# Kernel optimization log

Hardware: AMD Instinct MI355X
Metric: run time of the kernel (lower is better)

Reference implementation:

```python
import jax, jax.numpy as jnp
import numpy as np

IMG_W, IMG_H = 640, 480
OS = 8            # roialign output_size
SCALE = 1.0       # spatial_scale (boxes already mapped to feature coords)
ALIGNED = True
ALPHA = 1.0       # student-t alpha


def _roi_align_one(feat, boxes):
    # feat: [C, H, W]; boxes: [sn, 4] (x1, y1, x2, y2) in feature coords.
    # torchvision RoIAlign, sampling_ratio=1 (one sample at each bin center).
    C, H, W = feat.shape
    off = 0.5 if ALIGNED else 0.0
    x1 = boxes[:, 0] * SCALE - off
    y1 = boxes[:, 1] * SCALE - off
    x2 = boxes[:, 2] * SCALE - off
    y2 = boxes[:, 3] * SCALE - off
    bw = (x2 - x1) / OS   # bin width  [sn]
    bh = (y2 - y1) / OS   # bin height [sn]
    grid = jnp.arange(OS, dtype=feat.dtype) + 0.5
    xs = x1[:, None] + grid * bw[:, None]   # [sn, OS]
    ys = y1[:, None] + grid * bh[:, None]   # [sn, OS]
    X = jnp.broadcast_to(xs[:, None, :], (xs.shape[0], OS, OS))  # [sn,OS,OS]
    Y = jnp.broadcast_to(ys[:, :, None], (ys.shape[0], OS, OS))
    valid = (Y >= -1.0) & (Y <= H) & (X >= -1.0) & (X <= W)
    y = jnp.clip(Y, 0.0, H - 1)
    x = jnp.clip(X, 0.0, W - 1)
    y0f = jnp.floor(y); x0f = jnp.floor(x)
    y0 = y0f.astype(jnp.int32); x0 = x0f.astype(jnp.int32)
    y1i = jnp.minimum(y0 + 1, H - 1); x1i = jnp.minimum(x0 + 1, W - 1)
    ly = y - y0f; lx = x - x0f
    hy = 1.0 - ly; hx = 1.0 - lx
    def g(yi, xi):
        return feat[:, yi, xi]  # [C, sn, OS, OS]
    val = (hy * hx)[None] * g(y0, x0) + (hy * lx)[None] * g(y0, x1i) \
        + (ly * hx)[None] * g(y1i, x0) + (ly * lx)[None] * g(y1i, x1i)
    val = jnp.where(valid[None], val, 0.0)
    return jnp.transpose(val, (1, 0, 2, 3))  # [sn, C, OS, OS]


def setup_inputs() -> dict:
    key = jax.random.key(0)
    ks = jax.random.split(key, 10)
    B, SN, C, T, FY, FX = 16, 64, 480, 2, 60, 80
    NDF1, NDF2, K = 1024, 256, 64
    z = jax.random.normal(ks[0], (B, C, T, FY, FX), jnp.float32)
    # boxes in image pixel coords
    cx = jax.random.uniform(ks[1], (B, SN), minval=0.1, maxval=0.9) * IMG_W
    cy = jax.random.uniform(ks[2], (B, SN), minval=0.1, maxval=0.9) * IMG_H
    bw = jax.random.uniform(ks[3], (B, SN), minval=0.05, maxval=0.3) * IMG_W
    bh = jax.random.uniform(ks[4], (B, SN), minval=0.05, maxval=0.3) * IMG_H
    x1 = jnp.clip(cx - bw / 2, 0.0, IMG_W); x2 = jnp.clip(cx + bw / 2, 0.0, IMG_W)
    y1 = jnp.clip(cy - bh / 2, 0.0, IMG_H); y2 = jnp.clip(cy + bh / 2, 0.0, IMG_H)
    bboxs = jnp.stack([x1, y1, x2, y2], axis=-1).astype(jnp.float32)
    din = C * OS * OS
    w1 = jax.random.normal(ks[5], (NDF1, din), jnp.float32) * (din ** -0.5)
    b1 = jnp.zeros((NDF1,), jnp.float32)
    w2 = jax.random.normal(ks[6], (NDF2, NDF1), jnp.float32) * (NDF1 ** -0.5)
    b2 = jnp.zeros((NDF2,), jnp.float32)
    centroids = jax.random.normal(ks[7], (K, NDF2), jnp.float32)
    return {"z": z, "bboxs": bboxs, "w1": w1, "b1": b1, "w2": w2, "b2": b2,
            "centroids": centroids}


def reference(z, bboxs, w1, b1, w2, b2, centroids):
    B, C, T, fy, fx = z.shape
    sn = bboxs.shape[1]
    # scale image-space boxes to feature coords (per (x,y) pair as in torch code)
    sc = jnp.array([fx / IMG_W, fy / IMG_H], jnp.float32)
    bb = (bboxs.reshape(B, sn, 2, 2) * sc).reshape(B, sn, 4)
    bb = jnp.nan_to_num(bb)
    feat = z[:, :, -1]  # [B, C, fy, fx]
    pooled = jax.vmap(_roi_align_one)(feat, bb)  # [B, sn, C, OS, OS]
    flat = pooled.reshape(B * sn, -1)
    e = flat @ w1.T + b1
    e = e @ w2.T + b2
    zz = e.reshape(B, sn, -1)  # [B, sn, ndf2]
    # student-t soft assignment (faithful: L2 norm, not squared)
    z2 = jnp.sum(zz * zz, axis=-1, keepdims=True)          # [B,sn,1]
    c2 = jnp.sum(centroids * centroids, axis=-1)           # [K]
    zc = jnp.einsum('bsd,kd->bsk', zz, centroids)          # [B,sn,K]
    nrm = jnp.sqrt(jnp.maximum(z2 + c2 - 2.0 * zc, 0.0))
    s = ((1.0 + nrm) / ALPHA) ** (-(ALPHA + 1.0) / 2.0)
    s = s / jnp.sum(s, axis=-1, keepdims=True)
    c = jnp.argmax(s, axis=2)
    return zz, s, c
```

## Files before the change

### kernel.cpp

```cpp
#include <hip/hip_runtime.h>
#include <hip/hip_bf16.h>

static constexpr int B_  = 16;
static constexpr int SN_ = 64;
static constexpr int C_  = 480;
static constexpr int T_  = 2;
static constexpr int FY_ = 60;
static constexpr int FX_ = 80;
static constexpr int OS_ = 8;
static constexpr int DIN = 30720;
static constexpr int M_  = 1024;
static constexpr int N1_ = 1024;
static constexpr int N2_ = 256;
static constexpr int K_  = 64;
static constexpr int SPLITK = 32;
static constexpr int NCH_ZZ = (DIN / 64) / SPLITK;
static constexpr int NCH_FW = N1_ / 64;
static constexpr int CPB = 2;
static constexpr int IMG = FY_ * FX_;
static constexpr int NB_ROI = 16 * (C_ / CPB);
static constexpr int NB_W1T = (DIN / 64) * (N1_ / 64);
static constexpr int NB_W2P = N2_;

typedef __bf16 bf16x8 __attribute__((ext_vector_type(8)));
typedef float  f32x4  __attribute__((ext_vector_type(4)));
typedef unsigned int u32_as1 __attribute__((address_space(1)));
typedef unsigned int u32_as3 __attribute__((address_space(3)));

__device__ __forceinline__ float bf2f(unsigned short u) {
    union { unsigned int i; float f; } v; v.i = ((unsigned int)u) << 16; return v.f;
}
__device__ __forceinline__ unsigned short f2bf(float f) {
    unsigned int u = __float_as_uint(f);
    u = u + 0x7FFFu + ((u >> 16) & 1u);
    return (unsigned short)(u >> 16);
}
__device__ __forceinline__ void gll16(const void* g, void* l) {
    __builtin_amdgcn_global_load_lds((const u32_as1*)g, (u32_as3*)l, 16, 0, 0);
}

template<int NCHUNK, int SEG>
__device__ __forceinline__ void gemm_core(
    const unsigned short* __restrict__ Abase, long long Astride,
    const unsigned short* __restrict__ Bbase, long long Bstride,
    int k0, f32x4 (&acc)[4][2], unsigned short* L)
{
    const int t = threadIdx.x;
    const int w = t >> 6, lane = t & 63;
    const int rl8 = lane >> 3, slot = lane & 7;
    const int wm = w >> 2, wn = w & 3;
    const int fr = lane & 15, fg = lane >> 4;
    const int swz8 = (slot ^ rl8) * 8;

    long long arow[2], brow[2];
    int ci[2];
#pragma unroll
    for (int c = 0; c < 2; ++c) {
        ci[c] = w * 2 + c;
        const int row = ci[c] * 8 + rl8;
        arow[c] = (long long)row * Astride;
        brow[c] = (long long)row * Bstride;
    }

    auto stage = [&](int chunk, int par) {
        const int kin = k0 + chunk * 64;
        char* Lp = (char*)L + par * 65536;
#pragma unroll
        for (int c = 0; c < 2; ++c) {
            gll16(Abase + arow[c] + kin + swz8,       Lp + 0 * 16384 + ci[c] * 1024);
            gll16(Abase + arow[c] + SEG + kin + swz8, Lp + 1 * 16384 + ci[c] * 1024);
            gll16(Bbase + brow[c] + kin + swz8,       Lp + 2 * 16384 + ci[c] * 1024);
            gll16(Bbase + brow[c] + SEG + kin + swz8, Lp + 3 * 16384 + ci[c] * 1024);
        }
    };

    stage(0, 0);
    stage(1, 1);

    for (int it = 0; it < NCHUNK; ++it) {
        const int par = it & 1;
        if (it + 1 < NCHUNK) asm volatile("s_waitcnt vmcnt(8)" ::: "memory");
        else                 asm volatile("s_waitcnt vmcnt(0)" ::: "memory");
        __builtin_amdgcn_s_barrier();

        const char* Lp = (const char*)L + par * 65536;
        bf16x8 a[2][2][4], b[2][2][2];
#pragma unroll
        for (int hl = 0; hl < 2; ++hl)
#pragma unroll
            for (int ks = 0; ks < 2; ++ks)
#pragma unroll
                for (int mf = 0; mf < 4; ++mf) {
                    const int row = wm * 64 + mf * 16 + fr;
                    a[hl][ks][mf] = *reinterpret_cast<const bf16x8*>(
                        Lp + hl * 16384 + row * 128 + 16 * ((ks * 4 + fg) ^ (fr & 7)));
                }
#pragma unroll
        for (int hl = 0; hl < 2; ++hl)
#pragma unroll
            for (int ks = 0; ks < 2; ++ks)
#pragma unroll
                for (int nf = 0; nf < 2; ++nf) {
                    const int row = wn * 32 + nf * 16 + fr;
                    b[hl][ks][nf] = *reinterpret_cast<const bf16x8*>(
                        Lp + (2 + hl) * 16384 + row * 128 + 16 * ((ks * 4 + fg) ^ (fr & 7)));
                }
        asm volatile("s_waitcnt lgkmcnt(0)" ::: "memory");
        __builtin_amdgcn_sched_barrier(0);
        __builtin_amdgcn_s_barrier();
        __builtin_amdgcn_sched_barrier(0);
        if (it + 2 < NCHUNK) stage(it + 2, par);
        __builtin_amdgcn_sched_barrier(0);

        __builtin_amdgcn_s_setprio(1);
#pragma unroll
        for (int ks = 0; ks < 2; ++ks)
#pragma unroll
            for (int mf = 0; mf < 4; ++mf)
#pragma unroll
                for (int nf = 0; nf < 2; ++nf) {
                    acc[mf][nf] = __builtin_amdgcn_mfma_f32_16x16x32_bf16(
                        a[0][ks][mf], b[0][ks][nf], acc[mf][nf], 0, 0, 0);
                    acc[mf][nf] = __builtin_amdgcn_mfma_f32_16x16x32_bf16(
                        a[0][ks][mf], b[1][ks][nf], acc[mf][nf], 0, 0, 0);
                    acc[mf][nf] = __builtin_amdgcn_mfma_f32_16x16x32_bf16(
                        a[1][ks][mf], b[0][ks][nf], acc[mf][nf], 0, 0, 0);
                }
        __builtin_amdgcn_s_setprio(0);
    }
}

__global__ __launch_bounds__(256) void prep_kernel(
    const float* __restrict__ z, const float* __restrict__ bboxs,
    const float* __restrict__ w1, const float* __restrict__ w2,
    const float* __restrict__ b1, const float* __restrict__ b2,
    unsigned short* __restrict__ flat2, unsigned short* __restrict__ w1T2,
    unsigned short* __restrict__ w2cat, float* __restrict__ bf) {
    __shared__ __align__(16) char smem[39424];
    const int blk = blockIdx.x;
    const int t = threadIdx.x;

    if (blk < NB_ROI) {
        float* img = (float*)smem;
        float (*bxc)[4] = (float (*)[4])(smem + 38400);
        const int b  = blk / (C_ / CPB);
        const int cg = blk % (C_ / CPB);
        const float* zb = z + ((size_t)b * C_ + (size_t)cg * CPB) * (size_t)(T_ * IMG)
                            + (size_t)(T_ - 1) * IMG;
#pragma unroll
        for (int c = 0; c < CPB; ++c) {
            const float4* src = (const float4*)(zb + (size_t)c * (T_ * IMG));
            float4* dst = (float4*)(img + c * IMG);
            for (int i = t; i < IMG / 4; i += 256) dst[i] = src[i];
        }
        if (t < 64) {
            const float* bp = bboxs + ((size_t)b * 64 + t) * 4;
            const float v0 = bp[0], v1 = bp[1], v2 = bp[2], v3 = bp[3];
            bxc[t][0] = isnan(v0) ? 0.f : v0;
            bxc[t][1] = isnan(v1) ? 0.f : v1;
            bxc[t][2] = isnan(v2) ? 0.f : v2;
            bxc[t][3] = isnan(v3) ? 0.f : v3;
        }
        __syncthreads();

        const int p = t & 63, mh = t >> 6;
        const int gy = p >> 3, gx = p & 7;
        for (int mq = 0; mq < 16; ++mq) {
            const int m = mq * 4 + mh;
            const float x1 = bxc[m][0] * 0.125f - 0.5f;
            const float y1 = bxc[m][1] * 0.125f - 0.5f;
            const float x2 = bxc[m][2] * 0.125f - 0.5f;
            const float y2 = bxc[m][3] * 0.125f - 0.5f;
            const float bw = (x2 - x1) * (1.0f / OS_);
            const float bh = (y2 - y1) * (1.0f / OS_);
            const float X = x1 + ((float)gx + 0.5f) * bw;
            const float Y = y1 + ((float)gy + 0.5f) * bh;
            const bool valid = (Y >= -1.0f) && (Y <= (float)FY_) &&
                               (X >= -1.0f) && (X <= (float)FX_);
            const float yc = fminf(fmaxf(Y, 0.f), (float)(FY_ - 1));
            const float xc = fminf(fmaxf(X, 0.f), (float)(FX_ - 1));
            const float y0f = floorf(yc), x0f = floorf(xc);
            const int y0 = (int)y0f, x0 = (int)x0f;
            const int y1i = min(y0 + 1, FY_ - 1);
            const int x1i = min(x0 + 1, FX_ - 1);
            const float ly = yc - y0f, lx = xc - x0f;
            const float hy = 1.f - ly,  hx = 1.f - lx;
            float w00 = hy * hx, w01 = hy * lx, w10 = ly * hx, w11 = ly * lx;
            if (!valid) { w00 = 0.f; w01 = 0.f; w10 = 0.f; w11 = 0.f; }
            const int i00 = y0 * FX_ + x0, i01 = y0 * FX_ + x1i;
            const int i10 = y1i * FX_ + x0, i11 = y1i * FX_ + x1i;
            unsigned short* fo = flat2 + (size_t)(b * 64 + m) * (2 * DIN)
                                       + cg * (CPB * 64) + p;
#pragma unroll
            for (int c = 0; c < CPB; ++c) {
                const float* f = img + c * IMG;
                const float v = w00 * f[i00] + w01 * f[i01] + w10 * f[i10] + w11 * f[i11];
                const unsigned short hi = f2bf(v);
                const unsigned short lo = f2bf(v - bf2f(hi));
                fo[c * 64]       = hi;
                fo[DIN + c * 64] = lo;
            }
        }
    } else if (blk < NB_ROI + NB_W1T) {
        float (*L)[65] = (float (*)[65])smem;
        const int idx = blk - NB_ROI;
        const int q0 = (idx % (DIN / 64)) * 64, j0 = (idx / (DIN / 64)) * 64;
        const int tr = t >> 4, tc4 = (t & 15) * 4;
#pragma unroll
        for (int jj = 0; jj < 4; ++jj) {
            const int j = jj * 16 + tr;
            const float4 v = *(const float4*)(w1 + (size_t)(j0 + j) * DIN + q0 + tc4);
            L[j][tc4] = v.x; L[j][tc4 + 1] = v.y; L[j][tc4 + 2] = v.z; L[j][tc4 + 3] = v.w;
        }
        __syncthreads();
#pragma unroll
        for (int pass = 0; pass < 4; ++pass) {
            const int ql = pass * 16 + tr;
            const int jc = tc4;
            ushort4 h4, l4;
            float v0 = L[jc + 0][ql], v1 = L[jc + 1][ql], v2 = L[jc + 2][ql], v3 = L[jc + 3][ql];
            h4.x = f2bf(v0); l4.x = f2bf(v0 - bf2f(h4.x));
            h4.y = f2bf(v1); l4.y = f2bf(v1 - bf2f(h4.y));
            h4.z = f2bf(v2); l4.z = f2bf(v2 - bf2f(h4.z));
            h4.w = f2bf(v3); l4.w = f2bf(v3 - bf2f(h4.w));
            *(ushort4*)(w1T2 + (size_t)(q0 + ql) * 2048 + j0 + jc)        = h4;
            *(ushort4*)(w1T2 + (size_t)(q0 + ql) * 2048 + 1024 + j0 + jc) = l4;
        }
    } else {
        float* red = (float*)smem;
        const int p = blk - (NB_ROI + NB_W1T);
        float acc = 0.f;
#pragma unroll
        for (int j = t; j < N1_; j += 256) {
            const float v = w2[(size_t)p * N1_ + j];
            const unsigned short hi = f2bf(v);
            const unsigned short lo = f2bf(v - bf2f(hi));
            w2cat[(size_t)p * 2048 + j]        = hi;
            w2cat[(size_t)p * 2048 + 1024 + j] = lo;
            acc = fmaf(v, b1[j], acc);
        }
        red[t] = acc; __syncthreads();
        for (int s = 128; s > 0; s >>= 1) { if (t < s) red[t] += red[t + s]; __syncthreads(); }
        if (t == 0) bf[p] = red[0] + b2[p];
    }
}

__global__ __launch_bounds__(512, 1) void fusew_mfma(const unsigned short* __restrict__ w2cat,
                                                     const unsigned short* __restrict__ w1T2,
                                                     unsigned short* __restrict__ W2) {
    __shared__ __align__(16) unsigned short L[2 * 4 * 128 * 64];
    const int bid = blockIdx.x;
    const int xcd = bid & 7, j = bid >> 3;
    const int pb = j & 1;
    const int qb = xcd * 30 + (j >> 1);
    f32x4 acc[4][2];
#pragma unroll
    for (int i = 0; i < 4; ++i)
#pragma unroll
        for (int k = 0; k < 2; ++k) acc[i][k] = (f32x4){0.f, 0.f, 0.f, 0.f};

    gemm_core<NCH_FW, N1_>(w2cat + (long long)pb * 128 * 2048, 2048,
                           w1T2 + (long long)qb * 128 * 2048, 2048,
                           0, acc, L);

    const int t = threadIdx.x;
    const int w = t >> 6, lane = t & 63;
    const int wm = w >> 2, wn = w & 3;
    const int fr = lane & 15, fg = lane >> 4;
#pragma unroll
    for (int mf = 0; mf < 4; ++mf)
#pragma unroll
        for (int nf = 0; nf < 2; ++nf)
#pragma unroll
            for (int r = 0; r < 4; ++r) {
                const int p = pb * 128 + wm * 64 + mf * 16 + fg * 4 + r;
                const int q = qb * 128 + wn * 32 + nf * 16 + fr;
                const float v = acc[mf][nf][r];
                const unsigned short hi = f2bf(v);
                const unsigned short lo = f2bf(v - bf2f(hi));
                W2[(size_t)p * (2 * DIN) + q]       = hi;
                W2[(size_t)p * (2 * DIN) + DIN + q] = lo;
            }
}

__global__ __launch_bounds__(512, 1) void zz_mfma(const unsigned short* __restrict__ flat2,
                                                  const unsigned short* __restrict__ W2,
                                                  float* __restrict__ part) {
    __shared__ __align__(16) unsigned short L[2 * 4 * 128 * 64];
    const int bid = blockIdx.x;
    const int xcd = bid & 7, j = bid >> 3;
    const int mb = j & 7;
    const int pair = xcd * 8 + (j >> 3);
    const int nb = pair & 1, sp = pair >> 1;
    f32x4 acc[4][2];
#pragma unroll
    for (int i = 0; i < 4; ++i)
#pragma unroll
        for (int k = 0; k < 2; ++k) acc[i][k] = (f32x4){0.f, 0.f, 0.f, 0.f};

    gemm_core<NCH_ZZ, DIN>(flat2 + (long long)mb * 128 * (2 * DIN), 2 * DIN,
                           W2 + (long long)nb * 128 * (2 * DIN), 2 * DIN,
                           sp * (NCH_ZZ * 64), acc, L);

    float* po = part + (size_t)sp * (M_ * N2_);
    const int t = threadIdx.x;
    const int w = t >> 6, lane = t & 63;
    const int wm = w >> 2, wn = w & 3;
    const int fr = lane & 15, fg = lane >> 4;
#pragma unroll
    for (int mf = 0; mf < 4; ++mf)
#pragma unroll
        for (int nf = 0; nf < 2; ++nf)
#pragma unroll
            for (int r = 0; r < 4; ++r) {
                const int m = mb * 128 + wm * 64 + mf * 16 + fg * 4 + r;
                const int n = nb * 128 + wn * 32 + nf * 16 + fr;
                po[(size_t)m * N2_ + n] = acc[mf][nf][r];
            }
}

__global__ __launch_bounds__(256) void reduce_cluster_kernel(
    const float* __restrict__ part, const float* __restrict__ bf,
    const float* __restrict__ cent,
    float* __restrict__ out_zz, float* __restrict__ out_s, float* __restrict__ out_c) {
    __shared__ float row[N2_];
    const int m = blockIdx.x, t = threadIdx.x;
    float a = bf[t];
#pragma unroll
    for (int s = 0; s < SPLITK; ++s) a += part[(size_t)s * (M_ * N2_) + (size_t)m * N2_ + t];
    out_zz[(size_t)m * N2_ + t] = a;
    row[t] = a;
    __syncthreads();
    if (t < 64) {
        const float* cr = cent + (size_t)t * N2_;
        float dot = 0.f, c2 = 0.f, z2 = 0.f;
        for (int d = 0; d < N2_; ++d) {
            const float zv = row[d], cv = cr[d];
            dot = fmaf(zv, cv, dot);
            c2  = fmaf(cv, cv, c2);
            z2  = fmaf(zv, zv, z2);
        }
        const float nrm = sqrtf(fmaxf(z2 + c2 - 2.f * dot, 0.f));
        const float su = 1.0f / (1.0f + nrm);
        float ssum = su;
#pragma unroll
        for (int mk = 1; mk < 64; mk <<= 1) ssum += __shfl_xor(ssum, mk, 64);
        const float s = su / ssum;
        out_s[(size_t)m * 64 + t] = s;
        float bv = s; int bi = t;
#pragma unroll
        for (int mk = 1; mk < 64; mk <<= 1) {
            const float ov = __shfl_xor(bv, mk, 64);
            const int   oi = __shfl_xor(bi, mk, 64);
            if (ov > bv || (ov == bv && oi < bi)) { bv = ov; bi = oi; }
        }
        if (t == 0) out_c[m] = (float)bi;
    }
}

extern "C" void kernel_launch(void* const* d_in, const int* in_sizes, int n_in,
                              void* d_out, int out_size, void* d_ws, size_t ws_size,
                              hipStream_t stream) {
    const float* z     = (const float*)d_in[0];
    const float* bboxs = (const float*)d_in[1];
    const float* w1    = (const float*)d_in[2];
    const float* b1    = (const float*)d_in[3];
    const float* w2    = (const float*)d_in[4];
    const float* b2    = (const float*)d_in[5];
    const float* cent  = (const float*)d_in[6];
    float* out = (float*)d_out;
    float* out_zz = out;
    float* out_s  = out + (size_t)M_ * N2_;
    float* out_c  = out + (size_t)M_ * N2_ + (size_t)M_ * K_;

    char* ws = (char*)d_ws;
    unsigned short* w1T2   = (unsigned short*)(ws);
    unsigned short* flat2  = (unsigned short*)(ws + 125829120u);
    unsigned short* W2     = (unsigned short*)(ws + 251658240u);
    float*          part   = (float*)(ws + 283115520u);
    unsigned short* w2cat  = (unsigned short*)(ws + 316669952u);
    float*          bfused = (float*)(ws + 317718528u);

    prep_kernel<<<dim3(NB_ROI + NB_W1T + NB_W2P), dim3(256), 0, stream>>>(
        z, bboxs, w1, w2, b1, b2, flat2, w1T2, w2cat, bfused);
    fusew_mfma<<<dim3(480), dim3(512), 0, stream>>>(w2cat, w1T2, W2);
    zz_mfma<<<dim3(512), dim3(512), 0, stream>>>(flat2, W2, part);
    reduce_cluster_kernel<<<dim3(1024), dim3(256), 0, stream>>>(part, bfused, cent,
                                                                out_zz, out_s, out_c);
}
```

Measured before the change: 235.4 us.

## Merge ROI-align into fused-weight GEMM kernel and halve zz split-K

ROI-align pooling moves out of the prep kernel and into the same launch as the w2·w1 weight-fusion GEMM, so the two independent workloads share one grid. The ROI blocks now handle 4 channels with 512 threads. The zz GEMM split-K drops from 32 to 16, which halves the grid and the partial sums the reduce kernel must read. The tradeoff is that ROI blocks now hold 128KB of LDS, which limits occupancy, and zz has fewer, longer blocks.

Measured after the change: 264.9 us. 1.13x slower.

```diff
diff --git a/kernel.cpp b/kernel.cpp
--- a/kernel.cpp
+++ b/kernel.cpp
@@ -13,14 +13,15 @@
 static constexpr int N1_ = 1024;
 static constexpr int N2_ = 256;
 static constexpr int K_  = 64;
-static constexpr int SPLITK = 32;
+static constexpr int SPLITK = 16;
 static constexpr int NCH_ZZ = (DIN / 64) / SPLITK;
 static constexpr int NCH_FW = N1_ / 64;
-static constexpr int CPB = 2;
 static constexpr int IMG = FY_ * FX_;
-static constexpr int NB_ROI = 16 * (C_ / CPB);
 static constexpr int NB_W1T = (DIN / 64) * (N1_ / 64);
 static constexpr int NB_W2P = N2_;
+static constexpr int NB_FW   = 480;
+static constexpr int CPB2    = 4;
+static constexpr int NB_ROI2 = 16 * (C_ / CPB2);
 
 typedef __bf16 bf16x8 __attribute__((ext_vector_type(8)));
 typedef float  f32x4  __attribute__((ext_vector_type(4)));
@@ -130,28 +131,111 @@
     }
 }
 
-__global__ __launch_bounds__(256) void prep_kernel(
-    const float* __restrict__ z, const float* __restrict__ bboxs,
+__global__ __launch_bounds__(256) void prep1_kernel(
     const float* __restrict__ w1, const float* __restrict__ w2,
     const float* __restrict__ b1, const float* __restrict__ b2,
-    unsigned short* __restrict__ flat2, unsigned short* __restrict__ w1T2,
-    unsigned short* __restrict__ w2cat, float* __restrict__ bf) {
-    __shared__ __align__(16) char smem[39424];
+    unsigned short* __restrict__ w1T2, unsigned short* __restrict__ w2cat,
+    float* __restrict__ bf) {
+    __shared__ __align__(16) char smem[16640];
     const int blk = blockIdx.x;
     const int t = threadIdx.x;
 
-    if (blk < NB_ROI) {
+    if (blk < NB_W1T) {
+        float (*L)[65] = (float (*)[65])smem;
+        const int q0 = (blk % (DIN / 64)) * 64, j0 = (blk / (DIN / 64)) * 64;
+        const int tr = t >> 4, tc4 = (t & 15) * 4;
+#pragma unroll
+        for (int jj = 0; jj < 4; ++jj) {
+            const int j = jj * 16 + tr;
+            const float4 v = *(const float4*)(w1 + (size_t)(j0 + j) * DIN + q0 + tc4);
+            L[j][tc4] = v.x; L[j][tc4 + 1] = v.y; L[j][tc4 + 2] = v.z; L[j][tc4 + 3] = v.w;
+        }
+        __syncthreads();
+#pragma unroll
+        for (int pass = 0; pass < 4; ++pass) {
+            const int ql = pass * 16 + tr;
+            const int jc = tc4;
+            ushort4 h4, l4;
+            float v0 = L[jc + 0][ql], v1 = L[jc + 1][ql], v2 = L[jc + 2][ql], v3 = L[jc + 3][ql];
+            h4.x = f2bf(v0); l4.x = f2bf(v0 - bf2f(h4.x));
+            h4.y = f2bf(v1); l4.y = f2bf(v1 - bf2f(h4.y));
+            h4.z = f2bf(v2); l4.z = f2bf(v2 - bf2f(h4.z));
+            h4.w = f2bf(v3); l4.w = f2bf(v3 - bf2f(h4.w));
+            *(ushort4*)(w1T2 + (size_t)(q0 + ql) * 2048 + j0 + jc)        = h4;
+            *(ushort4*)(w1T2 + (size_t)(q0 + ql) * 2048 + 1024 + j0 + jc) = l4;
+        }
+    } else {
+        float* red = (float*)smem;
+        const int p = blk - NB_W1T;
+        float acc = 0.f;
+#pragma unroll
+        for (int j = t; j < N1_; j += 256) {
+            const float v = w2[(size_t)p * N1_ + j];
+            const unsigned short hi = f2bf(v);
+            const unsigned short lo = f2bf(v - bf2f(hi));
+            w2cat[(size_t)p * 2048 + j]        = hi;
+            w2cat[(size_t)p * 2048 + 1024 + j] = lo;
+            acc = fmaf(v, b1[j], acc);
+        }
+        red[t] = acc; __syncthreads();
+        for (int s = 128; s > 0; s >>= 1) { if (t < s) red[t] += red[t + s]; __syncthreads(); }
+        if (t == 0) bf[p] = red[0] + b2[p];
+    }
+}
+
+__global__ __launch_bounds__(512, 1) void mega2_kernel(
+    const float* __restrict__ z, const float* __restrict__ bboxs,
+    const unsigned short* __restrict__ w2cat, const unsigned short* __restrict__ w1T2,
+    unsigned short* __restrict__ W2, unsigned short* __restrict__ flat2) {
+    __shared__ __align__(16) char smem[131072];
+    __shared__ float bxc[64][4];
+    const int blk = blockIdx.x;
+    const int t = threadIdx.x;
+
+    if (blk < NB_FW) {
+        unsigned short* L = (unsigned short*)smem;
+        const int xcd = blk & 7, j = blk >> 3;
+        const int pb = j & 1;
+        const int qb = xcd * 30 + (j >> 1);
+        f32x4 acc[4][2];
+#pragma unroll
+        for (int i = 0; i < 4; ++i)
+#pragma unroll
+            for (int k = 0; k < 2; ++k) acc[i][k] = (f32x4){0.f, 0.f, 0.f, 0.f};
+
+        gemm_core<NCH_FW, N1_>(w2cat + (long long)pb * 128 * 2048, 2048,
+                               w1T2 + (long long)qb * 128 * 2048, 2048,
+                               0, acc, L);
+
+        const int w = t >> 6, lane = t & 63;
+        const int wm = w >> 2, wn = w & 3;
+        const int fr = lane & 15, fg = lane >> 4;
+#pragma unroll
+        for (int mf = 0; mf < 4; ++mf)
+#pragma unroll
+            for (int nf = 0; nf < 2; ++nf)
+#pragma unroll
+                for (int r = 0; r < 4; ++r) {
+                    const int p = pb * 128 + wm * 64 + mf * 16 + fg * 4 + r;
+                    const int q = qb * 128 + wn * 32 + nf * 16 + fr;
+                    const float v = acc[mf][nf][r];
+                    const unsigned short hi = f2bf(v);
+                    const unsigned short lo = f2bf(v - bf2f(hi));
+                    W2[(size_t)p * (2 * DIN) + q]       = hi;
+                    W2[(size_t)p * (2 * DIN) + DIN + q] = lo;
+                }
+    } else {
         float* img = (float*)smem;
-        float (*bxc)[4] = (float (*)[4])(smem + 38400);
-        const int b  = blk / (C_ / CPB);
-        const int cg = blk % (C_ / CPB);
-        const float* zb = z + ((size_t)b * C_ + (size_t)cg * CPB) * (size_t)(T_ * IMG)
+        const int idx = blk - NB_FW;
+        const int b  = idx / (C_ / CPB2);
+        const int cg = idx % (C_ / CPB2);
+        const float* zb = z + ((size_t)b * C_ + (size_t)cg * CPB2) * (size_t)(T_ * IMG)
                             + (size_t)(T_ - 1) * IMG;
 #pragma unroll
-        for (int c = 0; c < CPB; ++c) {
+        for (int c = 0; c < CPB2; ++c) {
             const float4* src = (const float4*)(zb + (size_t)c * (T_ * IMG));
             float4* dst = (float4*)(img + c * IMG);
-            for (int i = t; i < IMG / 4; i += 256) dst[i] = src[i];
+            for (int i = t; i < IMG / 4; i += 512) dst[i] = src[i];
         }
         if (t < 64) {
             const float* bp = bboxs + ((size_t)b * 64 + t) * 4;
@@ -165,8 +249,8 @@
 
         const int p = t & 63, mh = t >> 6;
         const int gy = p >> 3, gx = p & 7;
-        for (int mq = 0; mq < 16; ++mq) {
-            const int m = mq * 4 + mh;
+        for (int mq = 0; mq < 8; ++mq) {
+            const int m = mq * 8 + mh;
             const float x1 = bxc[m][0] * 0.125f - 0.5f;
             const float y1 = bxc[m][1] * 0.125f - 0.5f;
             const float x2 = bxc[m][2] * 0.125f - 0.5f;
@@ -190,9 +274,9 @@
             const int i00 = y0 * FX_ + x0, i01 = y0 * FX_ + x1i;
             const int i10 = y1i * FX_ + x0, i11 = y1i * FX_ + x1i;
             unsigned short* fo = flat2 + (size_t)(b * 64 + m) * (2 * DIN)
-                                       + cg * (CPB * 64) + p;
-#pragma unroll
-            for (int c = 0; c < CPB; ++c) {
+                                       + cg * (CPB2 * 64) + p;
+#pragma unroll
+            for (int c = 0; c < CPB2; ++c) {
                 const float* f = img + c * IMG;
                 const float v = w00 * f[i00] + w01 * f[i01] + w10 * f[i10] + w11 * f[i11];
                 const unsigned short hi = f2bf(v);
@@ -201,86 +285,7 @@
                 fo[DIN + c * 64] = lo;
             }
         }
-    } else if (blk < NB_ROI + NB_W1T) {
-        float (*L)[65] = (float (*)[65])smem;
-        const int idx = blk - NB_ROI;
-        const int q0 = (idx % (DIN / 64)) * 64, j0 = (idx / (DIN / 64)) * 64;
-        const int tr = t >> 4, tc4 = (t & 15) * 4;
-#pragma unroll
-        for (int jj = 0; jj < 4; ++jj) {
-            const int j = jj * 16 + tr;
-            const float4 v = *(const float4*)(w1 + (size_t)(j0 + j) * DIN + q0 + tc4);
-            L[j][tc4] = v.x; L[j][tc4 + 1] = v.y; L[j][tc4 + 2] = v.z; L[j][tc4 + 3] = v.w;
-        }
-        __syncthreads();
-#pragma unroll
-        for (int pass = 0; pass < 4; ++pass) {
-            const int ql = pass * 16 + tr;
-            const int jc = tc4;
-            ushort4 h4, l4;
-            float v0 = L[jc + 0][ql], v1 = L[jc + 1][ql], v2 = L[jc + 2][ql], v3 = L[jc + 3][ql];
-            h4.x = f2bf(v0); l4.x = f2bf(v0 - bf2f(h4.x));
-            h4.y = f2bf(v1); l4.y = f2bf(v1 - bf2f(h4.y));
-            h4.z = f2bf(v2); l4.z = f2bf(v2 - bf2f(h4.z));
-            h4.w = f2bf(v3); l4.w = f2bf(v3 - bf2f(h4.w));
-            *(ushort4*)(w1T2 + (size_t)(q0 + ql) * 2048 + j0 + jc)        = h4;
-            *(ushort4*)(w1T2 + (size_t)(q0 + ql) * 2048 + 1024 + j0 + jc) = l4;
-        }
-    } else {
-        float* red = (float*)smem;
-        const int p = blk - (NB_ROI + NB_W1T);
-        float acc = 0.f;
-#pragma unroll
-        for (int j = t; j < N1_; j += 256) {
-            const float v = w2[(size_t)p * N1_ + j];
-            const unsigned short hi = f2bf(v);
-            const unsigned short lo = f2bf(v - bf2f(hi));
-            w2cat[(size_t)p * 2048 + j]        = hi;
-            w2cat[(size_t)p * 2048 + 1024 + j] = lo;
-            acc = fmaf(v, b1[j], acc);
-        }
-        red[t] = acc; __syncthreads();
-        for (int s = 128; s > 0; s >>= 1) { if (t < s) red[t] += red[t + s]; __syncthreads(); }
-        if (t == 0) bf[p] = red[0] + b2[p];
-    }
-}
-
-__global__ __launch_bounds__(512, 1) void fusew_mfma(const unsigned short* __restrict__ w2cat,
-                                                     const unsigned short* __restrict__ w1T2,
-                                                     unsigned short* __restrict__ W2) {
-    __shared__ __align__(16) unsigned short L[2 * 4 * 128 * 64];
-    const int bid = blockIdx.x;
-    const int xcd = bid & 7, j = bid >> 3;
-    const int pb = j & 1;
-    const int qb = xcd * 30 + (j >> 1);
-    f32x4 acc[4][2];
-#pragma unroll
-    for (int i = 0; i < 4; ++i)
-#pragma unroll
-        for (int k = 0; k < 2; ++k) acc[i][k] = (f32x4){0.f, 0.f, 0.f, 0.f};
-
-    gemm_core<NCH_FW, N1_>(w2cat + (long long)pb * 128 * 2048, 2048,
-                           w1T2 + (long long)qb * 128 * 2048, 2048,
-                           0, acc, L);
-
-    const int t = threadIdx.x;
-    const int w = t >> 6, lane = t & 63;
-    const int wm = w >> 2, wn = w & 3;
-    const int fr = lane & 15, fg = lane >> 4;
-#pragma unroll
-    for (int mf = 0; mf < 4; ++mf)
-#pragma unroll
-        for (int nf = 0; nf < 2; ++nf)
-#pragma unroll
-            for (int r = 0; r < 4; ++r) {
-                const int p = pb * 128 + wm * 64 + mf * 16 + fg * 4 + r;
-                const int q = qb * 128 + wn * 32 + nf * 16 + fr;
-                const float v = acc[mf][nf][r];
-                const unsigned short hi = f2bf(v);
-                const unsigned short lo = f2bf(v - bf2f(hi));
-                W2[(size_t)p * (2 * DIN) + q]       = hi;
-                W2[(size_t)p * (2 * DIN) + DIN + q] = lo;
-            }
+    }
 }
 
 __global__ __launch_bounds__(512, 1) void zz_mfma(const unsigned short* __restrict__ flat2,
@@ -290,7 +295,7 @@
     const int bid = blockIdx.x;
     const int xcd = bid & 7, j = bid >> 3;
     const int mb = j & 7;
-    const int pair = xcd * 8 + (j >> 3);
+    const int pair = xcd * 4 + (j >> 3);
     const int nb = pair & 1, sp = pair >> 1;
     f32x4 acc[4][2];
 #pragma unroll
@@ -381,10 +386,11 @@
     unsigned short* w2cat  = (unsigned short*)(ws + 316669952u);
     float*          bfused = (float*)(ws + 317718528u);
 
-    prep_kernel<<<dim3(NB_ROI + NB_W1T + NB_W2P), dim3(256), 0, stream>>>(
-        z, bboxs, w1, w2, b1, b2, flat2, w1T2, w2cat, bfused);
-    fusew_mfma<<<dim3(480), dim3(512), 0, stream>>>(w2cat, w1T2, W2);
-    zz_mfma<<<dim3(512), dim3(512), 0, stream>>>(flat2, W2, part);
+    prep1_kernel<<<dim3(NB_W1T + NB_W2P), dim3(256), 0, stream>>>(
+        w1, w2, b1, b2, w1T2, w2cat, bfused);
+    mega2_kernel<<<dim3(NB_FW + NB_ROI2), dim3(512), 0, stream>>>(
+        z, bboxs, w2cat, w1T2, W2, flat2);
+    zz_mfma<<<dim3(256), dim3(512), 0, stream>>>(flat2, W2, part);
     reduce_cluster_kernel<<<dim3(1024), dim3(256), 0, stream>>>(part, bfused, cent,
                                                                 out_zz, out_s, out_c);
 }
```
